# Kernel optimization log

Hardware: AMD Instinct MI355X
Metric: run time of the kernel (lower is better)

Reference implementation:

```python
import jax, jax.numpy as jnp
import numpy as np
import math

LOG2PI = math.log(2.0 * math.pi)


def _gm_scale(m1, v1, m2, v2):
    # log-scale of product of two diagonal Gaussians (summed over last dim D)
    v1s = jnp.exp(2.0 * v1)
    v2s = jnp.exp(2.0 * v2)
    s = v1s + v2s
    ls = jnp.log(s)
    return (-0.5 * (LOG2PI + ls + (m1 - m2) ** 2 / s)).sum(-1)


def _gm_full(m1, v1, m2, v2):
    v1s = jnp.exp(2.0 * v1)
    v2s = jnp.exp(2.0 * v2)
    s = v1s + v2s
    ls = jnp.log(s)
    scale = (-0.5 * (LOG2PI + ls + (m1 - m2) ** 2 / s)).sum(-1)
    mu = (m1 * v2s + m2 * v1s) / s
    var = v1 + v2 - 0.5 * ls
    return scale, mu, var


def _child_part(cw, cm, cv, t_mu, t_var, side):
    # cw: (M,L,K); cm/cv: (M,L,K,D); t_mu/t_var: (L,L,L,C,D)
    if side == 'left':
        cm_b = cm[:, None, :, None, None, :, :]
        cv_b = cv[:, None, :, None, None, :, :]
        cw_b = cw[:, None, :, None, None, :]
    else:
        cm_b = cm[:, None, None, :, None, :, :]
        cv_b = cv[:, None, None, :, None, :, :]
        cw_b = cw[:, None, None, :, None, :]
    t_mu_b = t_mu[None, :, :, :, :, None, :]
    t_var_b = t_var[None, :, :, :, :, None, :]
    scale = _gm_scale(cm_b, cv_b, t_mu_b, t_var_b)  # (M,L,L,L,C,K)
    return jax.nn.logsumexp(scale + cw_b, axis=-1)  # (M,L,L,L,C)


def setup_inputs() -> dict:
    key = jax.random.key(0)
    ks = jax.random.split(key, 10)
    L, C, Ks, D = 5, 4, 4, 4
    n_leaves = 128
    N = 2 * n_leaves - 1  # complete binary tree, level order, leaves first
    f = jax.random.normal
    return {
        'state_weight': f(ks[0], (N, L, Ks), jnp.float32) * 0.5,
        'state_mu': f(ks[1], (N, L, Ks, D), jnp.float32) * 0.5,
        'state_var': f(ks[2], (N, L, Ks, D), jnp.float32) * 0.1,
        'trans_weight': f(ks[3], (L, L, L, C), jnp.float32) * 0.5,
        'trans_mu_p': f(ks[4], (L, L, L, C, D), jnp.float32) * 0.5,
        'trans_mu_lc': f(ks[5], (L, L, L, C, D), jnp.float32) * 0.5,
        'trans_mu_rc': f(ks[6], (L, L, L, C, D), jnp.float32) * 0.5,
        'trans_var_p': f(ks[7], (L, L, L, C, D), jnp.float32) * 0.1,
        'trans_var_lc': f(ks[8], (L, L, L, C, D), jnp.float32) * 0.1,
        'trans_var_rc': f(ks[9], (L, L, L, C, D), jnp.float32) * 0.1,
        'n_leaves': n_leaves,
    }


def reference(state_weight, state_mu, state_var, trans_weight, trans_mu_p,
              trans_mu_lc, trans_mu_rc, trans_var_p, trans_var_lc,
              trans_var_rc, n_leaves):
    L = trans_weight.shape[0]
    D = trans_mu_p.shape[-1]
    # inside pass over a complete binary tree, level by level
    w = state_weight[:n_leaves]      # (M,L,K)
    mu = state_mu[:n_leaves]         # (M,L,K,D)
    var = state_var[:n_leaves]
    off = n_leaves
    m = n_leaves // 2
    while m >= 1:
        left = _child_part(w[0::2], mu[0::2], var[0::2], trans_mu_lc, trans_var_lc, 'left')
        right = _child_part(w[1::2], mu[1::2], var[1::2], trans_mu_rc, trans_var_rc, 'right')
        cs = left + right + trans_weight[None]  # (m,L,L,L,C)
        sw = state_weight[off:off + m]          # (m,L,Ks)
        sm = state_mu[off:off + m]
        sv = state_var[off:off + m]
        sm_b = sm[:, :, None, None, :, None, :]   # (m,L,1,1,Ks,1,D)
        sv_b = sv[:, :, None, None, :, None, :]
        tp_mu = trans_mu_p[None, :, :, :, None, :, :]   # (1,L,L,L,1,C,D)
        tp_var = trans_var_p[None, :, :, :, None, :, :]
        scale, pmu, pvar = _gm_full(sm_b, sv_b, tp_mu, tp_var)  # (m,L,L,L,Ks,C)
        score = scale + cs[:, :, :, :, None, :] + sw[:, :, None, None, :, None]
        w = score.reshape(m, L, -1)  # K = L*L*Ks*C
        mu = jnp.broadcast_to(pmu, score.shape + (D,)).reshape(m, L, -1, D)
        var = jnp.broadcast_to(pvar, score.shape + (D,)).reshape(m, L, -1, D)
        off += m
        m //= 2
    return w[0], mu[0], var[0]
```

## Files before the change

kernel.cpp:

```cpp
#include <hip/hip_runtime.h>
#include <math.h>

#define L2PI4      7.3515082656373812f
#define HALF_L2PI4 3.6757541328186906f
#define LOG2E      1.4426950408889634f
#define LN2        0.6931471805599453f
#define C_HQ       0.7213475204444817f

__device__ __forceinline__ float frcp(float x)  { return __builtin_amdgcn_rcpf(x); }
__device__ __forceinline__ float frsq(float x)  { return __builtin_amdgcn_rsqf(x); }
__device__ __forceinline__ float flog2(float x) { return __builtin_amdgcn_logf(x); }
__device__ __forceinline__ float fexp2(float x) { return __builtin_amdgcn_exp2f(x); }

__global__ __launch_bounds__(256) void kAB32(
    const float* __restrict__ sw, const float* __restrict__ smu,
    const float* __restrict__ svar,
    const float* __restrict__ tw, const float4* __restrict__ tmp4,
    const float4* __restrict__ tvp4,
    const float4* __restrict__ tmL4, const float4* __restrict__ tvL4,
    const float4* __restrict__ tmR4, const float4* __restrict__ tvR4,
    float* __restrict__ lrC)
{
    int bid = blockIdx.x;
    int p = bid & 31, sl = bid >> 5;
    int side = (sl >= 25) ? 1 : 0;
    int r0 = sl - side * 25;
    int lc = r0 / 5, lp = r0 - lc * 5;
    int tid = threadIdx.x, lane = tid & 63, wave = tid >> 6;
    int cn = 2 * p + side;
    int node = 128 + cn;

    __shared__ float  s_lm[160], s_lve[160], s_lw2[40];
    __shared__ float  s_lr[200];
    __shared__ float  s_sm[16], s_sve[16], s_swl[4];
    __shared__ float4 s_fm[400], s_fv[400];
    __shared__ float  s_fw[400];
    __shared__ float4 s_tm[20], s_tv[20];
    __shared__ int    s_idx[20];

    if (tid < 160) {
        int which = tid >= 80, i = tid - which * 80;
        int nl = 2 * cn + which;
        s_lm[tid]  = smu[nl * 80 + i];
        s_lve[tid] = __expf(2.f * svar[nl * 80 + i]);
    } else if (tid < 200) {
        int t = tid - 160, which = t >= 20, i = t - which * 20;
        int nl = 2 * cn + which;
        s_lw2[t] = (sw[nl * 20 + i] - HALF_L2PI4) * LOG2E;
    } else if (tid < 216) {
        int i = tid - 200;
        s_sm[i]  = smu[node * 80 + lc * 16 + i];
        s_sve[i] = __expf(2.f * svar[node * 80 + lc * 16 + i]);
    } else if (tid < 220) {
        s_swl[tid - 216] = sw[node * 20 + lc * 4 + (tid - 216)];
    } else if (tid < 240) {
        int o = tid - 220, lo = o >> 2, c = o & 3;
        int idx = side ? (((lp * 5 + lo) * 5 + lc) * 4 + c)
                       : (((lp * 5 + lc) * 5 + lo) * 4 + c);
        s_idx[o] = idx;
        const float4* tmf = side ? tmR4 : tmL4;
        const float4* tvf = side ? tvR4 : tvL4;
        s_tm[o] = tmf[idx];
        float4 tvr = tvf[idx];
        s_tv[o] = make_float4(__expf(2.f * tvr.x), __expf(2.f * tvr.y),
                              __expf(2.f * tvr.z), __expf(2.f * tvr.w));
    }
    __syncthreads();

    for (int t = tid; t < 200; t += 256) {
        int which = t >= 100, q = t - which * 100;
        int r = q >> 2, c2 = q & 3;
        int llc = r / 5, lrc = r - llc * 5;
        int t4 = (lc * 25 + r) * 4 + c2;
        int lab = which ? lrc : llc;
        float4 tm  = (which ? tmR4 : tmL4)[t4];
        float4 tvr = (which ? tvR4 : tvL4)[t4];
        float4 tvo = make_float4(__expf(2.f * tvr.x), __expf(2.f * tvr.y),
                                 __expf(2.f * tvr.z), __expf(2.f * tvr.w));
        int sb = which * 80 + lab * 16;
        float vals[4];
        #pragma unroll
        for (int k = 0; k < 4; ++k) {
            int ci = sb + k * 4;
            float s0 = s_lve[ci+0] + tvo.x, s1 = s_lve[ci+1] + tvo.y;
            float s2 = s_lve[ci+2] + tvo.z, s3 = s_lve[ci+3] + tvo.w;
            float d0 = s_lm[ci+0] - tm.x, d1 = s_lm[ci+1] - tm.y;
            float d2 = s_lm[ci+2] - tm.z, d3 = s_lm[ci+3] - tm.w;
            float p01 = s0 * s1, p23 = s2 * s3;
            float q01 = fmaf(d0 * d0, s1, d1 * d1 * s0);
            float q23 = fmaf(d2 * d2, s3, d3 * d3 * s2);
            float P = p01 * p23;
            float Q = fmaf(q01, p23, q23 * p01);
            float rq = frsq(P);
            vals[k] = fmaf(-0.5f, flog2(P),
                           fmaf(-C_HQ, Q * rq * rq, s_lw2[which * 20 + lab * 4 + k]));
        }
        float M = fmaxf(fmaxf(vals[0], vals[1]), fmaxf(vals[2], vals[3]));
        float S = fexp2(vals[0]-M) + fexp2(vals[1]-M)
                + fexp2(vals[2]-M) + fexp2(vals[3]-M);
        s_lr[t] = (M + flog2(S)) * LN2;
    }
    __syncthreads();

    for (int e = tid; e < 400; e += 256) {
        int c2 = e & 3, ks = (e >> 2) & 3, r = e >> 4;
        int q = r * 4 + c2;
        int t4 = (lc * 25 + r) * 4 + c2;
        float csv = s_lr[q] + s_lr[100 + q] + tw[t4];
        float4 m2 = tmp4[t4];
        float4 vr = tvp4[t4];
        float4 e2 = make_float4(__expf(2.f * vr.x), __expf(2.f * vr.y),
                                __expf(2.f * vr.z), __expf(2.f * vr.w));
        float base2 = (csv + s_swl[ks] - L2PI4) * LOG2E;
        float v0 = s_sve[ks*4+0], v1 = s_sve[ks*4+1];
        float v2 = s_sve[ks*4+2], v3 = s_sve[ks*4+3];
        float m10 = s_sm[ks*4+0], m11 = s_sm[ks*4+1];
        float m12 = s_sm[ks*4+2], m13 = s_sm[ks*4+3];
        float s0 = v0 + e2.x, s1 = v1 + e2.y, s2 = v2 + e2.z, s3 = v3 + e2.w;
        float rs0 = frcp(s0), rs1 = frcp(s1), rs2 = frcp(s2), rs3 = frcp(s3);
        float d0 = m10 - m2.x, d1 = m11 - m2.y, d2 = m12 - m2.z, d3 = m13 - m2.w;
        float qs = fmaf(d0 * d0, rs0, fmaf(d1 * d1, rs1,
                   fmaf(d2 * d2, rs2, d3 * d3 * rs3)));
        float P = (s0 * s1) * (s2 * s3);
        float4 fm, fv;
        fm.x = fmaf(m10, e2.x, m2.x * v0) * rs0;  fv.x = v0 * e2.x * rs0;
        fm.y = fmaf(m11, e2.y, m2.y * v1) * rs1;  fv.y = v1 * e2.y * rs1;
        fm.z = fmaf(m12, e2.z, m2.z * v2) * rs2;  fv.z = v2 * e2.z * rs2;
        fm.w = fmaf(m13, e2.w, m2.w * v3) * rs3;  fv.w = v3 * e2.w * rs3;
        s_fm[e] = fm;
        s_fv[e] = fv;
        s_fw[e] = fmaf(-0.5f, flog2(P), fmaf(-C_HQ, qs, base2));
    }
    __syncthreads();

    float E[7], M;
    {
        float w[7];
        #pragma unroll
        for (int i = 0; i < 7; ++i) {
            int k = lane + (i << 6);
            w[i] = (k < 400) ? s_fw[k] : -1e30f;
        }
        M = w[0];
        #pragma unroll
        for (int i = 1; i < 7; ++i) M = fmaxf(M, w[i]);
        #pragma unroll
        for (int s = 32; s; s >>= 1) M = fmaxf(M, __shfl_xor(M, s));
        #pragma unroll
        for (int i = 0; i < 7; ++i) E[i] = fexp2(w[i] - M);
    }
    size_t lrb = (size_t)cn * 500;
    #pragma unroll
    for (int j = 0; j < 5; ++j) {
        int o = wave + 4 * j;
        float4 tmo = s_tm[o], tvo = s_tv[o];
        float S = 0.f;
        #pragma unroll
        for (int i = 0; i < 7; ++i) {
            int k = lane + (i << 6);
            int kc = k < 400 ? k : 0;
            float4 fm = s_fm[kc], fv = s_fv[kc];
            float ss0 = fv.x + tvo.x, ss1 = fv.y + tvo.y;
            float ss2 = fv.z + tvo.z, ss3 = fv.w + tvo.w;
            float dd0 = fm.x - tmo.x, dd1 = fm.y - tmo.y;
            float dd2 = fm.z - tmo.z, dd3 = fm.w - tmo.w;
            float p01 = ss0 * ss1, p23 = ss2 * ss3;
            float q01 = fmaf(dd0 * dd0, ss1, dd1 * dd1 * ss0);
            float q23 = fmaf(dd2 * dd2, ss3, dd3 * dd3 * ss2);
            float P = p01 * p23;
            float Q = fmaf(q01, p23, q23 * p01);
            float rq = frsq(P);
            S = fmaf(E[i] * rq, fexp2(-C_HQ * (Q * rq * rq)), S);
        }
        #pragma unroll
        for (int s = 32; s; s >>= 1) S += __shfl_xor(S, s);
        if (lane == 0) lrC[lrb + s_idx[o]] = (M + flog2(S)) * LN2;
    }
}

__global__ __launch_bounds__(256) void kAB(
    const float* __restrict__ lrP, float* __restrict__ lrC,
    const float* __restrict__ sw, const float* __restrict__ smu,
    const float* __restrict__ svar, int childOff,
    const float* __restrict__ tw, const float4* __restrict__ tmp4,
    const float4* __restrict__ tvp4,
    const float4* __restrict__ tmL4, const float4* __restrict__ tvL4,
    const float4* __restrict__ tmR4, const float4* __restrict__ tvR4,
    int log2m, int doFin, unsigned* __restrict__ cnt, float* __restrict__ out)
{
    int bid = blockIdx.x;
    int p = bid & ((1 << log2m) - 1), sl = bid >> log2m;
    int side = (sl >= 25) ? 1 : 0;
    int r0 = sl - side * 25;
    int lc = r0 / 5, lp = r0 - lc * 5;
    int tid = threadIdx.x, lane = tid & 63, wave = tid >> 6;
    int cn = 2 * p + side;
    int node = childOff + cn;

    __shared__ float  s_sm[16], s_sve[16], s_swl[4];
    __shared__ float4 s_fm[400], s_fv[400];
    __shared__ float  s_fw[400];
    __shared__ float4 s_tm[20], s_tv[20];
    __shared__ int    s_idx[20];
    __shared__ int    s_last;

    if (tid < 16) {
        s_sm[tid]  = smu[node * 80 + lc * 16 + tid];
        s_sve[tid] = __expf(2.f * svar[node * 80 + lc * 16 + tid]);
        if (tid < 4) s_swl[tid] = sw[node * 20 + lc * 4 + tid];
    }
    if (tid >= 64 && tid < 84) {
        int o = tid - 64, lo = o >> 2, c = o & 3;
        int idx = side ? (((lp * 5 + lo) * 5 + lc) * 4 + c)
                       : (((lp * 5 + lc) * 5 + lo) * 4 + c);
        s_idx[o] = idx;
        const float4* tmf = side ? tmR4 : tmL4;
        const float4* tvf = side ? tvR4 : tvL4;
        s_tm[o] = tmf[idx];
        float4 tvr = tvf[idx];
        s_tv[o] = make_float4(__expf(2.f * tvr.x), __expf(2.f * tvr.y),
                              __expf(2.f * tvr.z), __expf(2.f * tvr.w));
    }
    __syncthreads();

    const float* lrL = lrP + (size_t)(2 * cn) * 500;
    const float* lrR = lrP + (size_t)(2 * cn + 1) * 500;

    for (int e = tid; e < 400; e += 256) {
        int c2 = e & 3, ks = (e >> 2) & 3, r = e >> 4;
        int t4 = (lc * 25 + r) * 4 + c2;
        float csv = lrL[t4] + lrR[t4] + tw[t4];
        float4 m2 = tmp4[t4];
        float4 vr = tvp4[t4];
        float4 e2 = make_float4(__expf(2.f * vr.x), __expf(2.f * vr.y),
                                __expf(2.f * vr.z), __expf(2.f * vr.w));
        float base2 = (csv + s_swl[ks] - L2PI4) * LOG2E;
        float v0 = s_sve[ks*4+0], v1 = s_sve[ks*4+1];
        float v2 = s_sve[ks*4+2], v3 = s_sve[ks*4+3];
        float m10 = s_sm[ks*4+0], m11 = s_sm[ks*4+1];
        float m12 = s_sm[ks*4+2], m13 = s_sm[ks*4+3];
        float s0 = v0 + e2.x, s1 = v1 + e2.y, s2 = v2 + e2.z, s3 = v3 + e2.w;
        float rs0 = frcp(s0), rs1 = frcp(s1), rs2 = frcp(s2), rs3 = frcp(s3);
        float d0 = m10 - m2.x, d1 = m11 - m2.y, d2 = m12 - m2.z, d3 = m13 - m2.w;
        float qs = fmaf(d0 * d0, rs0, fmaf(d1 * d1, rs1,
                   fmaf(d2 * d2, rs2, d3 * d3 * rs3)));
        float P = (s0 * s1) * (s2 * s3);
        float4 fm, fv;
        fm.x = fmaf(m10, e2.x, m2.x * v0) * rs0;  fv.x = v0 * e2.x * rs0;
        fm.y = fmaf(m11, e2.y, m2.y * v1) * rs1;  fv.y = v1 * e2.y * rs1;
        fm.z = fmaf(m12, e2.z, m2.z * v2) * rs2;  fv.z = v2 * e2.z * rs2;
        fm.w = fmaf(m13, e2.w, m2.w * v3) * rs3;  fv.w = v3 * e2.w * rs3;
        s_fm[e] = fm;
        s_fv[e] = fv;
        s_fw[e] = fmaf(-0.5f, flog2(P), fmaf(-C_HQ, qs, base2));
    }
    __syncthreads();

    float E[7], M;
    {
        float w[7];
        #pragma unroll
        for (int i = 0; i < 7; ++i) {
            int k = lane + (i << 6);
            w[i] = (k < 400) ? s_fw[k] : -1e30f;
        }
        M = w[0];
        #pragma unroll
        for (int i = 1; i < 7; ++i) M = fmaxf(M, w[i]);
        #pragma unroll
        for (int s = 32; s; s >>= 1) M = fmaxf(M, __shfl_xor(M, s));
        #pragma unroll
        for (int i = 0; i < 7; ++i) E[i] = fexp2(w[i] - M);
    }

    size_t lrb = (size_t)cn * 500;
    #pragma unroll
    for (int j = 0; j < 5; ++j) {
        int o = wave + 4 * j;
        float4 tmo = s_tm[o], tvo = s_tv[o];
        float S = 0.f;
        #pragma unroll
        for (int i = 0; i < 7; ++i) {
            int k = lane + (i << 6);
            int kc = k < 400 ? k : 0;
            float4 fm = s_fm[kc], fv = s_fv[kc];
            float ss0 = fv.x + tvo.x, ss1 = fv.y + tvo.y;
            float ss2 = fv.z + tvo.z, ss3 = fv.w + tvo.w;
            float dd0 = fm.x - tmo.x, dd1 = fm.y - tmo.y;
            float dd2 = fm.z - tmo.z, dd3 = fm.w - tmo.w;
            float p01 = ss0 * ss1, p23 = ss2 * ss3;
            float q01 = fmaf(dd0 * dd0, ss1, dd1 * dd1 * ss0);
            float q23 = fmaf(dd2 * dd2, ss3, dd3 * dd3 * ss2);
            float P = p01 * p23;
            float Q = fmaf(q01, p23, q23 * p01);
            float rq = frsq(P);
            S = fmaf(E[i] * rq, fexp2(-C_HQ * (Q * rq * rq)), S);
        }
        #pragma unroll
        for (int s = 32; s; s >>= 1) S += __shfl_xor(S, s);
        if (lane == 0) lrC[lrb + s_idx[o]] = (M + flog2(S)) * LN2;
    }

    if (!doFin) return;
    __syncthreads();
    if (tid == 0) {
        __builtin_amdgcn_fence(__ATOMIC_RELEASE, "agent");
        unsigned old = __hip_atomic_fetch_add(cnt, 1u, __ATOMIC_RELAXED,
                                              __HIP_MEMORY_SCOPE_AGENT);
        s_last = (old == 49u);
    }
    __syncthreads();
    if (!s_last) return;
    __builtin_amdgcn_fence(__ATOMIC_ACQUIRE, "agent");

    float4* outmu4  = (float4*)(out + 2000);
    float4* outvar4 = (float4*)(out + 10000);
    for (int e = tid; e < 2000; e += 256) {
        int c = e & 3, ks = (e >> 2) & 3, r = e >> 4;
        int lrc = r % 5, r2 = r / 5, llc = r2 % 5, lp2 = r2 / 5;
        int t4 = ((lp2 * 5 + llc) * 5 + lrc) * 4 + c;
        float csv = lrC[t4] + lrC[500 + t4] + tw[t4];
        float4 m2 = tmp4[t4], v2 = tvp4[t4];
        float4 e2 = make_float4(__expf(2.f * v2.x), __expf(2.f * v2.y),
                                __expf(2.f * v2.z), __expf(2.f * v2.w));
        int sb = 254 * 80 + (lp2 * 4 + ks) * 4;
        float base = csv + sw[254 * 20 + lp2 * 4 + ks] - HALF_L2PI4;
        float scale = 0.f;
        float4 pmu, pvar;
        {
            float m1 = smu[sb+0], v1 = svar[sb+0], v1s = __expf(2.f * v1);
            float s = v1s + e2.x, rs = frcp(s), ls = flog2(s) * LN2, df = m1 - m2.x;
            scale += ls + df * df * rs;
            pmu.x = fmaf(m1, e2.x, m2.x * v1s) * rs; pvar.x = v1 + v2.x - 0.5f * ls;
        }
        {
            float m1 = smu[sb+1], v1 = svar[sb+1], v1s = __expf(2.f * v1);
            float s = v1s + e2.y, rs = frcp(s), ls = flog2(s) * LN2, df = m1 - m2.y;
            scale += ls + df * df * rs;
            pmu.y = fmaf(m1, e2.y, m2.y * v1s) * rs; pvar.y = v1 + v2.y - 0.5f * ls;
        }
        {
            float m1 = smu[sb+2], v1 = svar[sb+2], v1s = __expf(2.f * v1);
            float s = v1s + e2.z, rs = frcp(s), ls = flog2(s) * LN2, df = m1 - m2.z;
            scale += ls + df * df * rs;
            pmu.z = fmaf(m1, e2.z, m2.z * v1s) * rs; pvar.z = v1 + v2.z - 0.5f * ls;
        }
        {
            float m1 = smu[sb+3], v1 = svar[sb+3], v1s = __expf(2.f * v1);
            float s = v1s + e2.w, rs = frcp(s), ls = flog2(s) * LN2, df = m1 - m2.w;
            scale += ls + df * df * rs;
            pmu.w = fmaf(m1, e2.w, m2.w * v1s) * rs; pvar.w = v1 + v2.w - 0.5f * ls;
        }
        out[e]     = fmaf(-0.5f, scale, base);
        outmu4[e]  = pmu;
        outvar4[e] = pvar;
    }
}

extern "C" void kernel_launch(void* const* d_in, const int* in_sizes, int n_in,
                              void* d_out, int out_size, void* d_ws, size_t ws_size,
                              hipStream_t stream) {
    (void)in_sizes; (void)n_in; (void)out_size; (void)ws_size;
    const float* sw      = (const float*)d_in[0];
    const float* smu     = (const float*)d_in[1];
    const float* svar    = (const float*)d_in[2];
    const float* tw      = (const float*)d_in[3];
    const float* tmu_p   = (const float*)d_in[4];
    const float* tmu_lc  = (const float*)d_in[5];
    const float* tmu_rc  = (const float*)d_in[6];
    const float* tvar_p  = (const float*)d_in[7];
    const float* tvar_lc = (const float*)d_in[8];
    const float* tvar_rc = (const float*)d_in[9];

    float* ws   = (float*)d_ws;
    float* lrA  = ws;
    float* lrB  = lrA + 64000;
    unsigned* cnt = (unsigned*)(lrB + 64000);
    float* out  = (float*)d_out;

    hipMemsetAsync(cnt, 0, sizeof(unsigned), stream);

    hipLaunchKernelGGL(kAB32, dim3(1600), dim3(256), 0, stream,
                       sw, smu, svar, tw,
                       (const float4*)tmu_p, (const float4*)tvar_p,
                       (const float4*)tmu_lc, (const float4*)tvar_lc,
                       (const float4*)tmu_rc, (const float4*)tvar_rc,
                       lrA);

    const int childOffs[5] = {192, 224, 240, 248, 252};
    float* lrP = lrA;
    float* lrC = lrB;
    int li = 0;
    for (int lg = 4; lg >= 0; --lg, ++li) {
        int m = 1 << lg;
        int fin = (m == 1);
        hipLaunchKernelGGL(kAB, dim3(50 * m), dim3(256), 0, stream,
                           lrP, lrC,
                           sw, smu, svar, childOffs[li],
                           tw, (const float4*)tmu_p, (const float4*)tvar_p,
                           (const float4*)tmu_lc, (const float4*)tvar_lc,
                           (const float4*)tmu_rc, (const float4*)tvar_rc,
                           lg, fin, cnt, out);
        float* t = lrP; lrP = lrC; lrC = t;
    }
}
```

Measured before the change: 72.39 us.

## Fuse tree-level kernels into one persistent kernel with per-node counters

Replaces the five per-level kAB launches with a single kTail kernel of 800 blocks. Blocks at each level signal per-parent-node atomic counters and wait on them by spinning before computing the next level, so one dependency chain replaces four kernel boundaries. The counter reset moves into the first kernel, which drops the memset launch. This relies on all 800 blocks being co-resident so the spin-waits cannot deadlock, and a waiting block ties up a CU slot while it polls.

```diff
diff --git a/kernel.cpp b/kernel.cpp
--- a/kernel.cpp
+++ b/kernel.cpp
@@ -11,6 +11,149 @@
 __device__ __forceinline__ float frsq(float x)  { return __builtin_amdgcn_rsqf(x); }
 __device__ __forceinline__ float flog2(float x) { return __builtin_amdgcn_logf(x); }
 __device__ __forceinline__ float fexp2(float x) { return __builtin_amdgcn_exp2f(x); }
+
+__device__ __forceinline__ void arriveRel(unsigned* c, int tid) {
+    __syncthreads();
+    if (tid == 0) {
+        __builtin_amdgcn_fence(__ATOMIC_RELEASE, "agent");
+        __hip_atomic_fetch_add(c, 1u, __ATOMIC_RELAXED, __HIP_MEMORY_SCOPE_AGENT);
+    }
+}
+__device__ __forceinline__ void waitAcq(unsigned* c, int tid) {
+    if (tid == 0) {
+        long it = 0;
+        while (__hip_atomic_load(c, __ATOMIC_RELAXED, __HIP_MEMORY_SCOPE_AGENT) < 50u) {
+            __builtin_amdgcn_s_sleep(2);
+            if (++it > 1000000L) break;
+        }
+    }
+    __syncthreads();
+    __builtin_amdgcn_fence(__ATOMIC_ACQUIRE, "agent");
+}
+
+__device__ __forceinline__ void levelBody(
+    int u, int lg, int childOff,
+    const float* __restrict__ lrP, float* __restrict__ lrC,
+    const float* __restrict__ sw, const float* __restrict__ smu,
+    const float* __restrict__ svar,
+    const float* __restrict__ tw, const float4* __restrict__ tmp4,
+    const float4* __restrict__ tvp4,
+    const float4* __restrict__ tmL4, const float4* __restrict__ tvL4,
+    const float4* __restrict__ tmR4, const float4* __restrict__ tvR4,
+    int tid)
+{
+    __shared__ float  s_sm[16], s_sve[16], s_swl[4];
+    __shared__ float4 s_fm[400], s_fv[400];
+    __shared__ float  s_fw[400];
+    __shared__ float4 s_tm[20], s_tv[20];
+    __shared__ int    s_idx[20];
+
+    int p = u & ((1 << lg) - 1), sl = u >> lg;
+    int side = (sl >= 25) ? 1 : 0;
+    int r0 = sl - side * 25;
+    int lc = r0 / 5, lp = r0 - lc * 5;
+    int lane = tid & 63, wave = tid >> 6;
+    int cn = 2 * p + side;
+    int node = childOff + cn;
+
+    __syncthreads();
+    if (tid < 16) {
+        s_sm[tid]  = smu[node * 80 + lc * 16 + tid];
+        s_sve[tid] = __expf(2.f * svar[node * 80 + lc * 16 + tid]);
+        if (tid < 4) s_swl[tid] = sw[node * 20 + lc * 4 + tid];
+    }
+    if (tid >= 64 && tid < 84) {
+        int o = tid - 64, lo = o >> 2, c = o & 3;
+        int idx = side ? (((lp * 5 + lo) * 5 + lc) * 4 + c)
+                       : (((lp * 5 + lc) * 5 + lo) * 4 + c);
+        s_idx[o] = idx;
+        const float4* tmf = side ? tmR4 : tmL4;
+        const float4* tvf = side ? tvR4 : tvL4;
+        s_tm[o] = tmf[idx];
+        float4 tvr = tvf[idx];
+        s_tv[o] = make_float4(__expf(2.f * tvr.x), __expf(2.f * tvr.y),
+                              __expf(2.f * tvr.z), __expf(2.f * tvr.w));
+    }
+    __syncthreads();
+
+    const float* lrL = lrP + (size_t)(2 * cn) * 500;
+    const float* lrR = lrP + (size_t)(2 * cn + 1) * 500;
+
+    for (int e = tid; e < 400; e += 256) {
+        int c2 = e & 3, ks = (e >> 2) & 3, r = e >> 4;
+        int t4 = (lc * 25 + r) * 4 + c2;
+        float csv = lrL[t4] + lrR[t4] + tw[t4];
+        float4 m2 = tmp4[t4];
+        float4 vr = tvp4[t4];
+        float4 e2 = make_float4(__expf(2.f * vr.x), __expf(2.f * vr.y),
+                                __expf(2.f * vr.z), __expf(2.f * vr.w));
+        float base2 = (csv + s_swl[ks] - L2PI4) * LOG2E;
+        float v0 = s_sve[ks*4+0], v1 = s_sve[ks*4+1];
+        float v2 = s_sve[ks*4+2], v3 = s_sve[ks*4+3];
+        float m10 = s_sm[ks*4+0], m11 = s_sm[ks*4+1];
+        float m12 = s_sm[ks*4+2], m13 = s_sm[ks*4+3];
+        float s0 = v0 + e2.x, s1 = v1 + e2.y, s2 = v2 + e2.z, s3 = v3 + e2.w;
+        float rs0 = frcp(s0), rs1 = frcp(s1), rs2 = frcp(s2), rs3 = frcp(s3);
+        float d0 = m10 - m2.x, d1 = m11 - m2.y, d2 = m12 - m2.z, d3 = m13 - m2.w;
+        float qs = fmaf(d0 * d0, rs0, fmaf(d1 * d1, rs1,
+                   fmaf(d2 * d2, rs2, d3 * d3 * rs3)));
+        float P = (s0 * s1) * (s2 * s3);
+        float4 fm, fv;
+        fm.x = fmaf(m10, e2.x, m2.x * v0) * rs0;  fv.x = v0 * e2.x * rs0;
+        fm.y = fmaf(m11, e2.y, m2.y * v1) * rs1;  fv.y = v1 * e2.y * rs1;
+        fm.z = fmaf(m12, e2.z, m2.z * v2) * rs2;  fv.z = v2 * e2.z * rs2;
+        fm.w = fmaf(m13, e2.w, m2.w * v3) * rs3;  fv.w = v3 * e2.w * rs3;
+        s_fm[e] = fm;
+        s_fv[e] = fv;
+        s_fw[e] = fmaf(-0.5f, flog2(P), fmaf(-C_HQ, qs, base2));
+    }
+    __syncthreads();
+
+    float E[7], M;
+    {
+        float w[7];
+        #pragma unroll
+        for (int i = 0; i < 7; ++i) {
+            int k = lane + (i << 6);
+            w[i] = (k < 400) ? s_fw[k] : -1e30f;
+        }
+        M = w[0];
+        #pragma unroll
+        for (int i = 1; i < 7; ++i) M = fmaxf(M, w[i]);
+        #pragma unroll
+        for (int s = 32; s; s >>= 1) M = fmaxf(M, __shfl_xor(M, s));
+        #pragma unroll
+        for (int i = 0; i < 7; ++i) E[i] = fexp2(w[i] - M);
+    }
+
+    size_t lrb = (size_t)cn * 500;
+    #pragma unroll
+    for (int j = 0; j < 5; ++j) {
+        int o = wave + 4 * j;
+        float4 tmo = s_tm[o], tvo = s_tv[o];
+        float S = 0.f;
+        #pragma unroll
+        for (int i = 0; i < 7; ++i) {
+            int k = lane + (i << 6);
+            int kc = k < 400 ? k : 0;
+            float4 fm = s_fm[kc], fv = s_fv[kc];
+            float ss0 = fv.x + tvo.x, ss1 = fv.y + tvo.y;
+            float ss2 = fv.z + tvo.z, ss3 = fv.w + tvo.w;
+            float dd0 = fm.x - tmo.x, dd1 = fm.y - tmo.y;
+            float dd2 = fm.z - tmo.z, dd3 = fm.w - tmo.w;
+            float p01 = ss0 * ss1, p23 = ss2 * ss3;
+            float q01 = fmaf(dd0 * dd0, ss1, dd1 * dd1 * ss0);
+            float q23 = fmaf(dd2 * dd2, ss3, dd3 * dd3 * ss2);
+            float P = p01 * p23;
+            float Q = fmaf(q01, p23, q23 * p01);
+            float rq = frsq(P);
+            S = fmaf(E[i] * rq, fexp2(-C_HQ * (Q * rq * rq)), S);
+        }
+        #pragma unroll
+        for (int s = 32; s; s >>= 1) S += __shfl_xor(S, s);
+        if (lane == 0) lrC[lrb + s_idx[o]] = (M + flog2(S)) * LN2;
+    }
+}
 
 __global__ __launch_bounds__(256) void kAB32(
     const float* __restrict__ sw, const float* __restrict__ smu,
@@ -19,7 +162,7 @@
     const float4* __restrict__ tvp4,
     const float4* __restrict__ tmL4, const float4* __restrict__ tvL4,
     const float4* __restrict__ tmR4, const float4* __restrict__ tvR4,
-    float* __restrict__ lrC)
+    float* __restrict__ lrC, unsigned* __restrict__ cnt)
 {
     int bid = blockIdx.x;
     int p = bid & 31, sl = bid >> 5;
@@ -29,6 +172,10 @@
     int tid = threadIdx.x, lane = tid & 63, wave = tid >> 6;
     int cn = 2 * p + side;
     int node = 128 + cn;
+
+    if (bid == 0) {
+        for (int i = tid; i < 496; i += 256) cnt[i] = 0u;
+    }
 
     __shared__ float  s_lm[160], s_lve[160], s_lw2[40];
     __shared__ float  s_lr[200];
@@ -178,134 +325,52 @@
     }
 }
 
-__global__ __launch_bounds__(256) void kAB(
-    const float* __restrict__ lrP, float* __restrict__ lrC,
+__global__ __launch_bounds__(256) void kTail(
+    const float* __restrict__ lrA,
+    float* __restrict__ lrB, float* __restrict__ lr8, float* __restrict__ lr4,
+    float* __restrict__ lr2, float* __restrict__ lr1,
     const float* __restrict__ sw, const float* __restrict__ smu,
-    const float* __restrict__ svar, int childOff,
+    const float* __restrict__ svar,
     const float* __restrict__ tw, const float4* __restrict__ tmp4,
     const float4* __restrict__ tvp4,
     const float4* __restrict__ tmL4, const float4* __restrict__ tvL4,
     const float4* __restrict__ tmR4, const float4* __restrict__ tvR4,
-    int log2m, int doFin, unsigned* __restrict__ cnt, float* __restrict__ out)
+    unsigned* __restrict__ cnt, float* __restrict__ out)
 {
-    int bid = blockIdx.x;
-    int p = bid & ((1 << log2m) - 1), sl = bid >> log2m;
-    int side = (sl >= 25) ? 1 : 0;
-    int r0 = sl - side * 25;
-    int lc = r0 / 5, lp = r0 - lc * 5;
-    int tid = threadIdx.x, lane = tid & 63, wave = tid >> 6;
-    int cn = 2 * p + side;
-    int node = childOff + cn;
-
-    __shared__ float  s_sm[16], s_sve[16], s_swl[4];
-    __shared__ float4 s_fm[400], s_fv[400];
-    __shared__ float  s_fw[400];
-    __shared__ float4 s_tm[20], s_tv[20];
-    __shared__ int    s_idx[20];
-    __shared__ int    s_last;
-
-    if (tid < 16) {
-        s_sm[tid]  = smu[node * 80 + lc * 16 + tid];
-        s_sve[tid] = __expf(2.f * svar[node * 80 + lc * 16 + tid]);
-        if (tid < 4) s_swl[tid] = sw[node * 20 + lc * 4 + tid];
-    }
-    if (tid >= 64 && tid < 84) {
-        int o = tid - 64, lo = o >> 2, c = o & 3;
-        int idx = side ? (((lp * 5 + lo) * 5 + lc) * 4 + c)
-                       : (((lp * 5 + lc) * 5 + lo) * 4 + c);
-        s_idx[o] = idx;
-        const float4* tmf = side ? tmR4 : tmL4;
-        const float4* tvf = side ? tvR4 : tvL4;
-        s_tm[o] = tmf[idx];
-        float4 tvr = tvf[idx];
-        s_tv[o] = make_float4(__expf(2.f * tvr.x), __expf(2.f * tvr.y),
-                              __expf(2.f * tvr.z), __expf(2.f * tvr.w));
-    }
-    __syncthreads();
-
-    const float* lrL = lrP + (size_t)(2 * cn) * 500;
-    const float* lrR = lrP + (size_t)(2 * cn + 1) * 500;
-
-    for (int e = tid; e < 400; e += 256) {
-        int c2 = e & 3, ks = (e >> 2) & 3, r = e >> 4;
-        int t4 = (lc * 25 + r) * 4 + c2;
-        float csv = lrL[t4] + lrR[t4] + tw[t4];
-        float4 m2 = tmp4[t4];
-        float4 vr = tvp4[t4];
-        float4 e2 = make_float4(__expf(2.f * vr.x), __expf(2.f * vr.y),
-                                __expf(2.f * vr.z), __expf(2.f * vr.w));
-        float base2 = (csv + s_swl[ks] - L2PI4) * LOG2E;
-        float v0 = s_sve[ks*4+0], v1 = s_sve[ks*4+1];
-        float v2 = s_sve[ks*4+2], v3 = s_sve[ks*4+3];
-        float m10 = s_sm[ks*4+0], m11 = s_sm[ks*4+1];
-        float m12 = s_sm[ks*4+2], m13 = s_sm[ks*4+3];
-        float s0 = v0 + e2.x, s1 = v1 + e2.y, s2 = v2 + e2.z, s3 = v3 + e2.w;
-        float rs0 = frcp(s0), rs1 = frcp(s1), rs2 = frcp(s2), rs3 = frcp(s3);
-        float d0 = m10 - m2.x, d1 = m11 - m2.y, d2 = m12 - m2.z, d3 = m13 - m2.w;
-        float qs = fmaf(d0 * d0, rs0, fmaf(d1 * d1, rs1,
-                   fmaf(d2 * d2, rs2, d3 * d3 * rs3)));
-        float P = (s0 * s1) * (s2 * s3);
-        float4 fm, fv;
-        fm.x = fmaf(m10, e2.x, m2.x * v0) * rs0;  fv.x = v0 * e2.x * rs0;
-        fm.y = fmaf(m11, e2.y, m2.y * v1) * rs1;  fv.y = v1 * e2.y * rs1;
-        fm.z = fmaf(m12, e2.z, m2.z * v2) * rs2;  fv.z = v2 * e2.z * rs2;
-        fm.w = fmaf(m13, e2.w, m2.w * v3) * rs3;  fv.w = v3 * e2.w * rs3;
-        s_fm[e] = fm;
-        s_fv[e] = fv;
-        s_fw[e] = fmaf(-0.5f, flog2(P), fmaf(-C_HQ, qs, base2));
-    }
-    __syncthreads();
-
-    float E[7], M;
-    {
-        float w[7];
-        #pragma unroll
-        for (int i = 0; i < 7; ++i) {
-            int k = lane + (i << 6);
-            w[i] = (k < 400) ? s_fw[k] : -1e30f;
-        }
-        M = w[0];
-        #pragma unroll
-        for (int i = 1; i < 7; ++i) M = fmaxf(M, w[i]);
-        #pragma unroll
-        for (int s = 32; s; s >>= 1) M = fmaxf(M, __shfl_xor(M, s));
-        #pragma unroll
-        for (int i = 0; i < 7; ++i) E[i] = fexp2(w[i] - M);
-    }
-
-    size_t lrb = (size_t)cn * 500;
-    #pragma unroll
-    for (int j = 0; j < 5; ++j) {
-        int o = wave + 4 * j;
-        float4 tmo = s_tm[o], tvo = s_tv[o];
-        float S = 0.f;
-        #pragma unroll
-        for (int i = 0; i < 7; ++i) {
-            int k = lane + (i << 6);
-            int kc = k < 400 ? k : 0;
-            float4 fm = s_fm[kc], fv = s_fv[kc];
-            float ss0 = fv.x + tvo.x, ss1 = fv.y + tvo.y;
-            float ss2 = fv.z + tvo.z, ss3 = fv.w + tvo.w;
-            float dd0 = fm.x - tmo.x, dd1 = fm.y - tmo.y;
-            float dd2 = fm.z - tmo.z, dd3 = fm.w - tmo.w;
-            float p01 = ss0 * ss1, p23 = ss2 * ss3;
-            float q01 = fmaf(dd0 * dd0, ss1, dd1 * dd1 * ss0);
-            float q23 = fmaf(dd2 * dd2, ss3, dd3 * dd3 * ss2);
-            float P = p01 * p23;
-            float Q = fmaf(q01, p23, q23 * p01);
-            float rq = frsq(P);
-            S = fmaf(E[i] * rq, fexp2(-C_HQ * (Q * rq * rq)), S);
-        }
-        #pragma unroll
-        for (int s = 32; s; s >>= 1) S += __shfl_xor(S, s);
-        if (lane == 0) lrC[lrb + s_idx[o]] = (M + flog2(S)) * LN2;
-    }
-
-    if (!doFin) return;
+    int bid = blockIdx.x, tid = threadIdx.x;
+    __shared__ int s_last;
+
+    levelBody(bid, 4, 192, lrA, lrB, sw, smu, svar, tw, tmp4, tvp4,
+              tmL4, tvL4, tmR4, tvR4, tid);
+    arriveRel(&cnt[(0 + (bid & 15)) * 16], tid);
+    if (bid >= 400) return;
+    waitAcq(&cnt[(0 + 2 * (bid & 7) + (((bid >> 3) >= 25) ? 1 : 0)) * 16], tid);
+
+    levelBody(bid, 3, 224, lrB, lr8, sw, smu, svar, tw, tmp4, tvp4,
+              tmL4, tvL4, tmR4, tvR4, tid);
+    arriveRel(&cnt[(16 + (bid & 7)) * 16], tid);
+    if (bid >= 200) return;
+    waitAcq(&cnt[(16 + 2 * (bid & 3) + (((bid >> 2) >= 25) ? 1 : 0)) * 16], tid);
+
+    levelBody(bid, 2, 240, lr8, lr4, sw, smu, svar, tw, tmp4, tvp4,
+              tmL4, tvL4, tmR4, tvR4, tid);
+    arriveRel(&cnt[(24 + (bid & 3)) * 16], tid);
+    if (bid >= 100) return;
+    waitAcq(&cnt[(24 + 2 * (bid & 1) + (((bid >> 1) >= 25) ? 1 : 0)) * 16], tid);
+
+    levelBody(bid, 1, 248, lr4, lr2, sw, smu, svar, tw, tmp4, tvp4,
+              tmL4, tvL4, tmR4, tvR4, tid);
+    arriveRel(&cnt[(28 + (bid & 1)) * 16], tid);
+    if (bid >= 50) return;
+    waitAcq(&cnt[(28 + ((bid >= 25) ? 1 : 0)) * 16], tid);
+
+    levelBody(bid, 0, 252, lr2, lr1, sw, smu, svar, tw, tmp4, tvp4,
+              tmL4, tvL4, tmR4, tvR4, tid);
+
     __syncthreads();
     if (tid == 0) {
         __builtin_amdgcn_fence(__ATOMIC_RELEASE, "agent");
-        unsigned old = __hip_atomic_fetch_add(cnt, 1u, __ATOMIC_RELAXED,
+        unsigned old = __hip_atomic_fetch_add(&cnt[30 * 16], 1u, __ATOMIC_RELAXED,
                                               __HIP_MEMORY_SCOPE_AGENT);
         s_last = (old == 49u);
     }
@@ -319,7 +384,7 @@
         int c = e & 3, ks = (e >> 2) & 3, r = e >> 4;
         int lrc = r % 5, r2 = r / 5, llc = r2 % 5, lp2 = r2 / 5;
         int t4 = ((lp2 * 5 + llc) * 5 + lrc) * 4 + c;
-        float csv = lrC[t4] + lrC[500 + t4] + tw[t4];
+        float csv = lr1[t4] + lr1[500 + t4] + tw[t4];
         float4 m2 = tmp4[t4], v2 = tvp4[t4];
         float4 e2 = make_float4(__expf(2.f * v2.x), __expf(2.f * v2.y),
                                 __expf(2.f * v2.z), __expf(2.f * v2.w));
@@ -372,35 +437,28 @@
     const float* tvar_lc = (const float*)d_in[8];
     const float* tvar_rc = (const float*)d_in[9];
 
-    float* ws   = (float*)d_ws;
-    float* lrA  = ws;
-    float* lrB  = lrA + 64000;
-    unsigned* cnt = (unsigned*)(lrB + 64000);
-    float* out  = (float*)d_out;
-
-    hipMemsetAsync(cnt, 0, sizeof(unsigned), stream);
+    float* ws  = (float*)d_ws;
+    float* lrA = ws;
+    float* lrB = lrA + 64000;
+    float* lr8 = lrB + 64000;
+    float* lr4 = lr8 + 8000;
+    float* lr2 = lr4 + 4000;
+    float* lr1 = lr2 + 2000;
+    unsigned* cnt = (unsigned*)(lr1 + 1000);
+    float* out = (float*)d_out;
 
     hipLaunchKernelGGL(kAB32, dim3(1600), dim3(256), 0, stream,
                        sw, smu, svar, tw,
                        (const float4*)tmu_p, (const float4*)tvar_p,
                        (const float4*)tmu_lc, (const float4*)tvar_lc,
                        (const float4*)tmu_rc, (const float4*)tvar_rc,
-                       lrA);
-
-    const int childOffs[5] = {192, 224, 240, 248, 252};
-    float* lrP = lrA;
-    float* lrC = lrB;
-    int li = 0;
-    for (int lg = 4; lg >= 0; --lg, ++li) {
-        int m = 1 << lg;
-        int fin = (m == 1);
-        hipLaunchKernelGGL(kAB, dim3(50 * m), dim3(256), 0, stream,
-                           lrP, lrC,
-                           sw, smu, svar, childOffs[li],
-                           tw, (const float4*)tmu_p, (const float4*)tvar_p,
-                           (const float4*)tmu_lc, (const float4*)tvar_lc,
-                           (const float4*)tmu_rc, (const float4*)tvar_rc,
-                           lg, fin, cnt, out);
-        float* t = lrP; lrP = lrC; lrC = t;
-    }
-}
+                       lrA, cnt);
+
+    hipLaunchKernelGGL(kTail, dim3(800), dim3(256), 0, stream,
+                       lrA, lrB, lr8, lr4, lr2, lr1,
+                       sw, smu, svar, tw,
+                       (const float4*)tmu_p, (const float4*)tvar_p,
+                       (const float4*)tmu_lc, (const float4*)tvar_lc,
+                       (const float4*)tmu_rc, (const float4*)tvar_rc,
+                       cnt, out);
+}
```

Measured after the change: 102.4 us. 1.41x slower.
